# Performance work log

Measured on AMD Instinct MI355X. Metric: run time of the kernel, lower is better.

Reference implementation:

```python
import jax, jax.numpy as jnp
import numpy as np

H = 512          # hidden_dim
D = 128          # input_dim
L = 8            # output_dim == NUMLABELS
T = 64           # encoder time steps per frame-feature sequence
W = 240          # WINDOWWIDTH (encoder batch dim, one element per frame)
CTX = W // 4     # 60 attention positions
NSTEPS = W // 8


def _lstm(x, Wih, Whh, bih, bhh):
    """PyTorch-convention LSTM (gate order i,f,g,o). x: (T,B,Din) -> (outputs (T,B,H), final h (B,H))."""
    B = x.shape[1]
    Hh = Whh.shape[1]
    xp = jnp.einsum('tbd,gd->tbg', x, Wih) + bih + bhh  # fold both biases
    def step(carry, g):
        h, c = carry
        g = g + h @ Whh.T
        i, f, gg, o = jnp.split(g, 4, axis=-1)
        c = jax.nn.sigmoid(f) * c + jax.nn.sigmoid(i) * jnp.tanh(gg)
        h = jax.nn.sigmoid(o) * jnp.tanh(c)
        return (h, c), h
    z = jnp.zeros((B, Hh), x.dtype)
    (hT, _), hs = jax.lax.scan(step, (z, z), xp)
    return hs, hT


def _forward(data, enc_Wih, enc_Whh, enc_bih, enc_bhh,
             p1f_Wih, p1f_Whh, p1f_bih, p1f_bhh, p1b_Wih, p1b_Whh, p1b_bih, p1b_bhh,
             p2f_Wih, p2f_Whh, p2f_bih, p2f_bhh, p2b_Wih, p2b_Whh, p2b_bih, p2b_bhh,
             attn_W, attn_b, comb_W, comb_b,
             gru_Wih, gru_Whh, gru_bih, gru_bhh, out_W, out_b):
    # --- encoder: per-frame LSTM over T steps, keep final hidden per frame ---
    _, h_enc = _lstm(data, enc_Wih, enc_Whh, enc_bih, enc_bhh)          # (W, H)
    # --- pyramidal bi-LSTM 1: pairs of frames ---
    x1 = h_enc.reshape(W // 2, 1, 2 * H)
    f1, _ = _lstm(x1, p1f_Wih, p1f_Whh, p1f_bih, p1f_bhh)
    b1, _ = _lstm(x1[::-1], p1b_Wih, p1b_Whh, p1b_bih, p1b_bhh)
    # --- pyramidal bi-LSTM 2 ---
    x2 = jnp.concatenate([f1, b1[::-1]], axis=-1).reshape(W // 4, 1, 4 * H)
    f2, h2T = _lstm(x2, p2f_Wih, p2f_Whh, p2f_bih, p2f_bhh)
    b2, _ = _lstm(x2[::-1], p2b_Wih, p2b_Whh, p2b_bih, p2b_bhh)
    ctx = jnp.concatenate([f2, b2[::-1]], axis=-1).reshape(CTX, 2 * H)  # (60, 2H)
    h = h2T[0]                                   # forward-direction final hidden, (H,)
    inp0 = jnp.zeros((L,), data.dtype).at[L - 1].set(1.0)  # one_hot(NOLABEL)

    def dec_step(carry, _):
        inp, h = carry
        aw = jax.nn.softmax(attn_W @ jnp.concatenate([inp, h]) + attn_b)    # (60,)
        applied = aw @ ctx                                                   # (2H,)
        o = jax.nn.relu(comb_W @ jnp.concatenate([inp, applied]) + comb_b)  # (H,)
        # PyTorch GRU cell (gate order r,z,n)
        gi = gru_Wih @ o + gru_bih
        gh = gru_Whh @ h + gru_bhh
        ir, iz, inn = jnp.split(gi, 3)
        hr, hz, hn = jnp.split(gh, 3)
        r = jax.nn.sigmoid(ir + hr)
        z = jax.nn.sigmoid(iz + hz)
        n = jnp.tanh(inn + r * hn)
        h_new = (1.0 - z) * n + z * h
        logp = jax.nn.log_softmax(out_W @ h_new + out_b)                     # (L,)
        return (logp, h_new), logp  # prediction feeds back as next input (y=None path)

    _, outputs = jax.lax.scan(dec_step, (inp0, h), None, length=NSTEPS)
    return outputs  # (30, L)


def setup_inputs() -> dict:
    key = jax.random.key(0)
    ks = iter(jax.random.split(key, 64))
    def mk(*shape):
        return (jax.random.normal(next(ks), shape) * 0.05).astype(jnp.float32)
    d = {"data": jax.random.normal(next(ks), (T, W, D), dtype=jnp.float32)}
    d.update(enc_Wih=mk(4 * H, D), enc_Whh=mk(4 * H, H), enc_bih=mk(4 * H), enc_bhh=mk(4 * H))
    for p, din in (("p1f", 2 * H), ("p1b", 2 * H), ("p2f", 4 * H), ("p2b", 4 * H)):
        d[p + "_Wih"] = mk(4 * H, din)
        d[p + "_Whh"] = mk(4 * H, H)
        d[p + "_bih"] = mk(4 * H)
        d[p + "_bhh"] = mk(4 * H)
    d.update(attn_W=mk(CTX, H + L), attn_b=mk(CTX), comb_W=mk(H, 2 * H + L), comb_b=mk(H),
             gru_Wih=mk(3 * H, H), gru_Whh=mk(3 * H, H), gru_bih=mk(3 * H), gru_bhh=mk(3 * H),
             out_W=mk(L, H), out_b=mk(L))
    return d


def reference(data, enc_Wih, enc_Whh, enc_bih, enc_bhh,
              p1f_Wih, p1f_Whh, p1f_bih, p1f_bhh, p1b_Wih, p1b_Whh, p1b_bih, p1b_bhh,
              p2f_Wih, p2f_Whh, p2f_bih, p2f_bhh, p2b_Wih, p2b_Whh, p2b_bih, p2b_bhh,
              attn_W, attn_b, comb_W, comb_b,
              gru_Wih, gru_Whh, gru_bih, gru_bhh, out_W, out_b):
    return _forward(data, enc_Wih, enc_Whh, enc_bih, enc_bhh,
                    p1f_Wih, p1f_Whh, p1f_bih, p1f_bhh, p1b_Wih, p1b_Whh, p1b_bih, p1b_bhh,
                    p2f_Wih, p2f_Whh, p2f_bih, p2f_bhh, p2b_Wih, p2b_Whh, p2b_bih, p2b_bhh,
                    attn_W, attn_b, comb_W, comb_b,
                    gru_Wih, gru_Whh, gru_bih, gru_bhh, out_W, out_b)
```

## Files before the change

### kernel.cpp

```cpp
#include <hip/hip_runtime.h>
#include <math.h>


typedef __attribute__((ext_vector_type(8))) short short8;
typedef __attribute__((ext_vector_type(4))) float floatx4;
typedef unsigned long long ull;

__device__ __forceinline__ float sigf(float x) { return 1.f / (1.f + __expf(-x)); }
__device__ __forceinline__ float tanh_f(float x) {
    float e = __expf(2.f * x);
    return 1.f - 2.f / (e + 1.f);
}
__device__ __forceinline__ unsigned short f2b(float x) {
    unsigned u = __float_as_uint(x);
    unsigned r = (u + 0x7FFFu + ((u >> 16) & 1u)) >> 16;
    return (unsigned short)r;
}

__device__ __forceinline__ float gld(const float* p) {
    return __hip_atomic_load(p, __ATOMIC_RELAXED, __HIP_MEMORY_SCOPE_AGENT);
}
__device__ __forceinline__ void gst(float* p, float v) {
    __hip_atomic_store(p, v, __ATOMIC_RELAXED, __HIP_MEMORY_SCOPE_AGENT);
}
__device__ __forceinline__ ull gldll(const ull* p) {
    return __hip_atomic_load(p, __ATOMIC_RELAXED, __HIP_MEMORY_SCOPE_AGENT);
}
__device__ __forceinline__ void gstll(ull* p, ull v) {
    __hip_atomic_store(p, v, __ATOMIC_RELAXED, __HIP_MEMORY_SCOPE_AGENT);
}
__device__ __forceinline__ ull packfe(float d, int ep) {
    return ((ull)(unsigned)ep << 32) | (ull)__float_as_uint(d);
}
__device__ __forceinline__ float lowf(ull v) { return __uint_as_float((unsigned)v); }

__global__ void init_k(float* __restrict__ ws) {
    for (int i = blockIdx.x * blockDim.x + threadIdx.x; i < 256000; i += gridDim.x * blockDim.x)
        ws[i] = 0.f;
}

__global__ void __launch_bounds__(256, 1) enc_all(
    const float* __restrict__ data,
    const float* __restrict__ Wih, const float* __restrict__ Whh,
    const float* __restrict__ bih, const float* __restrict__ bhh,
    ull* __restrict__ hbufF,
    float* __restrict__ henc)
{
    __shared__ short act2[20 * 64 * 8];
    __shared__ float gw[4][640];
    __shared__ float cs[512];
    __shared__ short hw[4][16][8];
    __shared__ float biasL[4][4][8];

    const int tid = threadIdx.x;
    const int fg = blockIdx.x >> 4, ds = blockIdx.x & 15;
    const int w = tid >> 6, lane = tid & 63;
    const int n = lane & 15, q = lane >> 4;

    short8 bfrag[2][20];
#pragma unroll
    for (int nt = 0; nt < 2; ++nt) {
        int rr = nt * 16 + n;
        int g = rr >> 3, dp = rr & 7;
        int grow = g * 512 + ds * 32 + w * 8 + dp;
#pragma unroll
        for (int kt = 0; kt < 20; ++kt) {
            int k0 = kt * 32 + q * 8;
            const float* src = (k0 < 512) ? (Whh + (size_t)grow * 512 + k0)
                                          : (Wih + (size_t)grow * 128 + (k0 - 512));
            float4 lo = *(const float4*)src;
            float4 hi = *(const float4*)(src + 4);
            short8 bf;
            bf[0] = (short)f2b(lo.x); bf[1] = (short)f2b(lo.y);
            bf[2] = (short)f2b(lo.z); bf[3] = (short)f2b(lo.w);
            bf[4] = (short)f2b(hi.x); bf[5] = (short)f2b(hi.y);
            bf[6] = (short)f2b(hi.z); bf[7] = (short)f2b(hi.w);
            bfrag[nt][kt] = bf;
        }
    }
    if (tid < 128) {
        int w2 = tid >> 5, rr = tid & 31;
        int g = rr >> 3, dp = rr & 7;
        int grow = g * 512 + ds * 32 + w2 * 8 + dp;
        biasL[w2][g][dp] = bih[grow] + bhh[grow];
    }
    for (int i = tid; i < 512; i += 256) cs[i] = 0.f;
    __syncthreads();

    unsigned* a2u = (unsigned*)act2;

    for (int t = 0; t < 64; ++t) {
        const int kt2 = tid >> 6, l2 = tid & 63, f2v = l2 & 15, q2 = l2 >> 4;
        const float* xs = data + ((size_t)t * 240 + fg * 16 + f2v) * 128 + kt2 * 32 + q2 * 8;
        float4 lo = *(const float4*)xs;
        float4 hi = *(const float4*)(xs + 4);

        {
            const ull* hsrc = hbufF + (size_t)((t & 1) * 15 + fg) * 4096;
            ull v[16];
            for (;;) {
                bool ok = true;
#pragma unroll
                for (int k2 = 0; k2 < 16; ++k2) {
                    v[k2] = gldll(hsrc + tid + 256 * k2);
                    ok &= ((int)(v[k2] >> 32) == t);
                }
                if (ok) break;
                __builtin_amdgcn_s_sleep(1);
            }
#pragma unroll
            for (int k2 = 0; k2 < 16; ++k2)
                a2u[tid + 256 * k2] = (unsigned)v[k2];
        }
        {
            short8 xp;
            xp[0] = (short)f2b(lo.x); xp[1] = (short)f2b(lo.y);
            xp[2] = (short)f2b(lo.z); xp[3] = (short)f2b(lo.w);
            xp[4] = (short)f2b(hi.x); xp[5] = (short)f2b(hi.y);
            xp[6] = (short)f2b(hi.z); xp[7] = (short)f2b(hi.w);
            *(short8*)&act2[((16 + kt2) * 64 + l2) * 8] = xp;
        }
        __syncthreads();

        floatx4 acc0 = {0.f, 0.f, 0.f, 0.f};
        floatx4 acc1 = {0.f, 0.f, 0.f, 0.f};
#pragma unroll
        for (int kt = 0; kt < 20; ++kt) {
            short8 a = *(short8*)&act2[(kt * 64 + lane) * 8];
            acc0 = __builtin_amdgcn_mfma_f32_16x16x32_bf16(a, bfrag[0][kt], acc0, 0, 0, 0);
            acc1 = __builtin_amdgcn_mfma_f32_16x16x32_bf16(a, bfrag[1][kt], acc1, 0, 0, 0);
        }
        *(floatx4*)&gw[w][(0 * 16 + n) * 20 + 4 * q] = acc0;
        *(floatx4*)&gw[w][(1 * 16 + n) * 20 + 4 * q] = acc1;

        int nb = (t + 1) & 1;
#pragma unroll
        for (int it = 0; it < 2; ++it) {
            int f = lane & 15, dp = q + 4 * it;
            float gi = gw[w][(0 * 8 + dp) * 20 + f] + biasL[w][0][dp];
            float gf = gw[w][(1 * 8 + dp) * 20 + f] + biasL[w][1][dp];
            float gg = gw[w][(2 * 8 + dp) * 20 + f] + biasL[w][2][dp];
            float go = gw[w][(3 * 8 + dp) * 20 + f] + biasL[w][3][dp];
            int ci = f * 32 + w * 8 + dp;
            float cc = cs[ci];
            float cn = sigf(gf) * cc + sigf(gi) * tanh_f(gg);
            float hn = sigf(go) * tanh_f(cn);
            cs[ci] = cn;
            hw[w][f][dp] = (short)f2b(hn);
            if (t == 63)
                gst(&henc[(size_t)(fg * 16 + f) * 512 + ds * 32 + w * 8 + dp], hn);
        }
        if (lane < 16) {
            const unsigned* hwu = (const unsigned*)&hw[w][lane][0];
            ull* dst = hbufF + (size_t)(nb * 15 + fg) * 4096 + (ds * 64 + w * 16 + lane) * 4;
            const ull ep = ((ull)(unsigned)(t + 1)) << 32;
#pragma unroll
            for (int r = 0; r < 4; ++r)
                gstll(dst + r, ep | (ull)hwu[r]);
        }
        __syncthreads();
    }
}

__global__ void __launch_bounds__(256) gemm_xp2(
    const float* __restrict__ A, int M, int K, int halfgrid,
    const float* __restrict__ WvF, const float* __restrict__ baF,
    const float* __restrict__ bbF, float* __restrict__ CF,
    const float* __restrict__ WvB, const float* __restrict__ baB,
    const float* __restrict__ bbB, float* __restrict__ CB)
{
    __shared__ float At[16][66];
    __shared__ float Wt[128][66];
    const int tid = threadIdx.x;
    int bgl = blockIdx.x;
    const int rev = (bgl >= halfgrid) ? 1 : 0;
    if (rev) bgl -= halfgrid;
    const float* Wv = rev ? WvB : WvF;
    const float* ba = rev ? baB : baF;
    const float* bb = rev ? bbB : bbF;
    float* C        = rev ? CB : CF;

    const int nt = bgl & 15, mt = bgl >> 4;
    const int rp = tid >> 2, fq = tid & 3;
    const int lr0 = 2 * rp, lr1 = lr0 + 1;
    const int n0 = nt * 128 + lr0, n1 = n0 + 1;

    float acc0[4], acc1[4];
    {
        float b0 = ba[n0] + bb[n0], b1 = ba[n1] + bb[n1];
#pragma unroll
        for (int j = 0; j < 4; ++j) { acc0[j] = b0; acc1[j] = b1; }
    }

    for (int kt = 0; kt < K; kt += 64) {
        {
            int f = tid >> 4, c4 = tid & 15;
            int m = mt * 16 + f;
            float4 v = make_float4(0.f, 0.f, 0.f, 0.f);
            if (m < M) {
                int ar = rev ? (M - 1 - m) : m;
                v = ((const float4*)(A + (size_t)ar * K + kt))[c4];
            }
            At[f][c4 * 4 + 0] = v.x; At[f][c4 * 4 + 1] = v.y;
            At[f][c4 * 4 + 2] = v.z; At[f][c4 * 4 + 3] = v.w;
        }
        for (int i = tid; i < 2048; i += 256) {
            int lr = i >> 4, c4 = i & 15;
            float4 v = ((const float4*)(Wv + (size_t)(nt * 128 + lr) * K + kt))[c4];
            Wt[lr][c4 * 4 + 0] = v.x; Wt[lr][c4 * 4 + 1] = v.y;
            Wt[lr][c4 * 4 + 2] = v.z; Wt[lr][c4 * 4 + 3] = v.w;
        }
        __syncthreads();
        const float2* w0p = (const float2*)(&Wt[lr0][0]);
        const float2* w1p = (const float2*)(&Wt[lr1][0]);
#pragma unroll 8
        for (int kh = 0; kh < 32; ++kh) {
            float2 w0 = w0p[kh], w1 = w1p[kh];
#pragma unroll
            for (int j = 0; j < 4; ++j) {
                float2 av = ((const float2*)(&At[4 * fq + j][0]))[kh];
                acc0[j] += w0.x * av.x + w0.y * av.y;
                acc1[j] += w1.x * av.x + w1.y * av.y;
            }
        }
        __syncthreads();
    }
#pragma unroll
    for (int j = 0; j < 4; ++j) {
        int m = mt * 16 + 4 * fq + j;
        if (m < M) {
            C[(size_t)m * 2048 + n0] = acc0[j];
            C[(size_t)m * 2048 + n1] = acc1[j];
        }
    }
}

__global__ void __launch_bounds__(256, 1) pyr_rec(
    const float* __restrict__ xpF, const float* __restrict__ xpB,
    const float* __restrict__ WhhF, const float* __restrict__ WhhB,
    ull* __restrict__ hp,
    float* __restrict__ outF, float* __restrict__ outB,
    int steps)
{
    const int tid = threadIdx.x;
    const int dir = blockIdx.x >> 6, blk = blockIdx.x & 63;
    const float* xp  = dir ? xpB : xpF;
    const float* Whh = dir ? WhhB : WhhF;
    float* outp = dir ? outB : outF;
    ull* hpd = hp + (size_t)dir * 1024;

    __shared__ __align__(16) float hcur[512];
    __shared__ float red[32][9];
    __shared__ float gv[32];

    const int lr = tid & 31, seg = tid >> 5;
    const int grow = (lr >> 3) * 512 + blk * 8 + (lr & 7);
    float4 wl4[16];
#pragma unroll
    for (int j = 0; j < 16; ++j)
        wl4[j] = *(const float4*)&Whh[(size_t)grow * 512 + 4 * seg + 32 * j];

    const int growx = (tid >> 3) * 512 + blk * 8 + (tid & 7);
    float creg = 0.f;
    __syncthreads();

    for (int t = 0; t < steps; ++t) {
        float xg = 0.f;
        if (tid < 32) xg = xp[(size_t)t * 2048 + growx];
        {
            const ull* base = hpd + (size_t)(t & 1) * 512;
            ull v0 = gldll(base + tid), v1 = gldll(base + tid + 256);
            while (((int)(v0 >> 32) != t) | ((int)(v1 >> 32) != t)) {
                __builtin_amdgcn_s_sleep(1);
                v0 = gldll(base + tid);
                v1 = gldll(base + tid + 256);
            }
            hcur[tid]       = lowf(v0);
            hcur[tid + 256] = lowf(v1);
        }
        __syncthreads();

        float a = 0.f;
#pragma unroll
        for (int j = 0; j < 16; ++j) {
            float4 w = wl4[j];
            float4 h4 = *(const float4*)&hcur[4 * seg + 32 * j];
            a += w.x*h4.x + w.y*h4.y + w.z*h4.z + w.w*h4.w;
        }
        red[lr][seg] = a;
        __syncthreads();

        if (tid < 32) {
            float g = xg;
#pragma unroll
            for (int s2 = 0; s2 < 8; ++s2) g += red[tid][s2];
            gv[tid] = g;
        }
        __syncthreads();
        if (tid < 8) {
            float i_ = sigf(gv[tid]), f_ = sigf(gv[8 + tid]);
            float g_ = tanh_f(gv[16 + tid]), o_ = sigf(gv[24 + tid]);
            creg = f_ * creg + i_ * g_;
            float hn = o_ * tanh_f(creg);
            int d = blk * 8 + tid;
            gstll(&hpd[((t + 1) & 1) * 512 + d], packfe(hn, t + 1));
            int row = dir ? (steps - 1 - t) : t;
            outp[(size_t)row * 512 + d] = hn;
        }
        __syncthreads();
    }
}

__global__ void x2_assemble(const float* __restrict__ f1, const float* __restrict__ b1o,
                            float* __restrict__ x2)
{
    int j = blockIdx.x;
    for (int k = threadIdx.x; k < 2048; k += 256) {
        int q = k >> 9, r = k & 511;
        const float* src = (q & 1) ? b1o : f1;
        int row = 2 * j + (q >> 1);
        x2[(size_t)j * 2048 + k] = src[(size_t)row * 512 + r];
    }
}

__global__ void ctx_k(const float* __restrict__ f2, const float* __restrict__ b2o,
                      float* __restrict__ ctx, ull* __restrict__ hdec_p)
{
    int j = blockIdx.x;
    for (int k = threadIdx.x; k < 1024; k += 256)
        ctx[(size_t)j * 1024 + k] = (k < 512) ? f2[(size_t)j * 512 + k]
                                              : b2o[(size_t)j * 512 + k - 512];
    if (j == 0) {
        for (int i = threadIdx.x; i < 512; i += 256)
            hdec_p[i] = packfe(f2[59 * 512 + i], 0);
    }
}

__global__ void __launch_bounds__(256) precomp_M(
    const float* __restrict__ comb_W,
    const float* __restrict__ ctx,
    float* __restrict__ MgT)
{
    __shared__ float cw[8 * 1024];
    const int tid = threadIdx.x, d0 = blockIdx.x * 8;
    for (int i = tid; i < 2048; i += 256) {
        int r = i >> 8, c4 = i & 255;
        float4 v = *(const float4*)&comb_W[(size_t)(d0 + r) * 1032 + 8 + 4 * c4];
        *(float4*)&cw[r * 1024 + 4 * c4] = v;
    }
    __syncthreads();
    for (int o = tid; o < 480; o += 256) {
        int dl = o / 60, j = o % 60;
        const float4* cp = (const float4*)&cw[dl * 1024];
        const float4* xp = (const float4*)(ctx + (size_t)j * 1024);
        float a = 0.f;
#pragma unroll 4
        for (int k = 0; k < 256; ++k) {
            float4 w = cp[k], x = xp[k];
            a += w.x * x.x + w.y * x.y + w.z * x.z + w.w * x.w;
        }
        MgT[(size_t)j * 512 + (d0 + dl)] = a;
    }
}

__global__ void __launch_bounds__(512, 1) dec_k(
    const float* __restrict__ attn_W, const float* __restrict__ attn_b,
    const float* __restrict__ comb_W, const float* __restrict__ comb_b,
    const float* __restrict__ gWih, const float* __restrict__ gWhh,
    const float* __restrict__ gbih, const float* __restrict__ gbhh,
    const float* __restrict__ outW, const float* __restrict__ outb,
    const float* __restrict__ MgT,
    ull* __restrict__ hdec_p,
    float* __restrict__ dout)
{
    const int tid = threadIdx.x, bid = blockIdx.x;
    const int lane = tid & 63, wv = tid >> 6;
    const int dbase = bid * 8;

    __shared__ float M2T[68][512];
    __shared__ __align__(16) float hL[520];
    __shared__ __align__(16) float xl[512];
    __shared__ __align__(16) float awx[68];
    __shared__ float zd[8], zh[64];
    __shared__ float ghl[24], gil[24];
    __shared__ float biasg[24], biasi[24];
    __shared__ float cbL[512];
    __shared__ float attnbL[64], outbL[8];

    const int rg = tid >> 4, sg = tid & 15;
    const int rz = tid >> 3, szz = tid & 7;

    float4 wo2[2];
    float4 wg8[8], wi8[8];
    float4 wzh[16];
    float4 wip[2];
    {
        const float* wp = outW + (size_t)wv * 512 + 4 * lane;
        wo2[0] = *(const float4*)wp;
        wo2[1] = *(const float4*)(wp + 256);
    }
    {
        int rr = (rg < 24) ? rg : 23;
        size_t grow = (size_t)((rr >> 3) * 512 + dbase + (rr & 7)) * 512 + 4 * sg;
#pragma unroll
        for (int i = 0; i < 8; ++i) {
            wg8[i] = *(const float4*)&gWhh[grow + 64 * i];
            wi8[i] = *(const float4*)&gWih[grow + 64 * i];
        }
    }
    {
        int rr = (rz < 60) ? rz : 59;
        size_t base = (size_t)rr * 520 + 8 + 4 * szz;
#pragma unroll
        for (int i = 0; i < 16; ++i)
            wzh[i] = *(const float4*)&attn_W[base + 32 * i];
    }
    {
        int rr = (tid < 60) ? tid : 59;
        wip[0] = *(const float4*)&attn_W[(size_t)rr * 520 + 0];
        wip[1] = *(const float4*)&attn_W[(size_t)rr * 520 + 4];
    }
    if (tid < 24) {
        int g2 = (tid >> 3) * 512 + dbase + (tid & 7);
        biasg[tid] = gbhh[g2];
        biasi[tid] = gbih[g2];
    }
    cbL[tid] = comb_b[tid];
    if (tid < 64) attnbL[tid] = (tid < 60) ? attn_b[tid] : 0.f;
    if (tid < 8) outbL[tid] = outb[tid];
    for (int i = tid; i < 7680; i += 512) {
        int j = i >> 7, c4 = i & 127;
        *(float4*)&M2T[j][4 * c4] = *(const float4*)&MgT[(size_t)j * 512 + 4 * c4];
    }
    for (int i = tid; i < 4096; i += 512) {
        int r = i >> 3, c = i & 7;
        M2T[60 + c][r] = comb_W[(size_t)r * 1032 + c];
    }
    __syncthreads();

    for (int s = 0; s < 30; ++s) {
        {
            const ull* hs = hdec_p + (size_t)(s & 1) * 512;
            ull v0 = gldll(hs + tid);
            while ((int)(v0 >> 32) != s) {
                __builtin_amdgcn_s_sleep(1);
                v0 = gldll(hs + tid);
            }
            hL[tid] = lowf(v0);
        }
        __syncthreads();

        {
            float a = 0.f;
            float4 h0 = *(const float4*)&hL[4 * lane];
            float4 h1 = *(const float4*)&hL[4 * lane + 256];
            a += wo2[0].x*h0.x + wo2[0].y*h0.y + wo2[0].z*h0.z + wo2[0].w*h0.w;
            a += wo2[1].x*h1.x + wo2[1].y*h1.y + wo2[1].z*h1.z + wo2[1].w*h1.w;
#pragma unroll
            for (int off = 32; off; off >>= 1) a += __shfl_xor(a, off);
            if (lane == 0) zd[wv] = a;
        }
        {
            float a = 0.f;
#pragma unroll
            for (int i = 0; i < 8; ++i) {
                float4 w = wg8[i];
                float4 h4 = *(const float4*)&hL[4 * sg + 64 * i];
                a += w.x*h4.x + w.y*h4.y + w.z*h4.z + w.w*h4.w;
            }
            a += __shfl_xor(a, 1); a += __shfl_xor(a, 2);
            a += __shfl_xor(a, 4); a += __shfl_xor(a, 8);
            if (sg == 0 && rg < 24) ghl[rg] = a;
        }
        {
            float a = 0.f;
#pragma unroll
            for (int i = 0; i < 16; ++i) {
                float4 w = wzh[i];
                float4 h4 = *(const float4*)&hL[4 * szz + 32 * i];
                a += w.x*h4.x + w.y*h4.y + w.z*h4.z + w.w*h4.w;
            }
            a += __shfl_xor(a, 1); a += __shfl_xor(a, 2); a += __shfl_xor(a, 4);
            if (szz == 0 && rz < 60) zh[rz] = a;
        }
        __syncthreads();

        if (wv == 0) {
            if (lane < 8) {
                float v;
                if (s > 0) {
                    float a = zd[lane] + outbL[lane];
                    float m = a;
                    m = fmaxf(m, __shfl_xor(m, 1));
                    m = fmaxf(m, __shfl_xor(m, 2));
                    m = fmaxf(m, __shfl_xor(m, 4));
                    float e = __expf(a - m);
                    float ss2 = e;
                    ss2 += __shfl_xor(ss2, 1);
                    ss2 += __shfl_xor(ss2, 2);
                    ss2 += __shfl_xor(ss2, 4);
                    v = a - m - __logf(ss2);
                    if (bid == 0) dout[(s - 1) * 8 + lane] = v;
                } else {
                    v = (lane == 7) ? 1.f : 0.f;
                }
                awx[60 + lane] = v;
            }
            float z = -1e30f;
            if (lane < 60) {
                z = zh[lane] + attnbL[lane]
                  + wip[0].x * awx[60] + wip[0].y * awx[61]
                  + wip[0].z * awx[62] + wip[0].w * awx[63]
                  + wip[1].x * awx[64] + wip[1].y * awx[65]
                  + wip[1].z * awx[66] + wip[1].w * awx[67];
            }
            float m = z;
#pragma unroll
            for (int off = 32; off; off >>= 1) m = fmaxf(m, __shfl_xor(m, off));
            float e = (lane < 60) ? __expf(z - m) : 0.f;
            float ss2 = e;
#pragma unroll
            for (int off = 32; off; off >>= 1) ss2 += __shfl_xor(ss2, off);
            if (lane < 60) awx[lane] = e / ss2;
        }
        __syncthreads();

        {
            float a = cbL[tid];
#pragma unroll 4
            for (int k = 0; k < 68; ++k)
                a += M2T[k][tid] * awx[k];
            xl[tid] = fmaxf(a, 0.f);
        }
        __syncthreads();

        {
            float a = 0.f;
#pragma unroll
            for (int i = 0; i < 8; ++i) {
                float4 w = wi8[i];
                float4 o4 = *(const float4*)&xl[4 * sg + 64 * i];
                a += w.x*o4.x + w.y*o4.y + w.z*o4.z + w.w*o4.w;
            }
            a += __shfl_xor(a, 1); a += __shfl_xor(a, 2);
            a += __shfl_xor(a, 4); a += __shfl_xor(a, 8);
            if (sg == 0 && rg < 24) gil[rg] = a;
        }
        __syncthreads();

        if (tid < 8) {
            float gh0 = biasg[tid] + ghl[tid];
            float gh1 = biasg[8 + tid] + ghl[8 + tid];
            float gh2 = biasg[16 + tid] + ghl[16 + tid];
            float gi0 = biasi[tid] + gil[tid];
            float gi1 = biasi[8 + tid] + gil[8 + tid];
            float gi2 = biasi[16 + tid] + gil[16 + tid];
            float r_ = sigf(gi0 + gh0);
            float z_ = sigf(gi1 + gh1);
            float n_ = tanh_f(gi2 + r_ * gh2);
            float hnew = (1.f - z_) * n_ + z_ * hL[dbase + tid];
            gstll(&hdec_p[(size_t)((s + 1) & 1) * 512 + dbase + tid], packfe(hnew, s + 1));
        }
        __syncthreads();
    }

    if (bid == 0) {
        {
            const ull* hs = hdec_p + (size_t)(30 & 1) * 512;
            ull v0 = gldll(hs + tid);
            while ((int)(v0 >> 32) != 30) {
                __builtin_amdgcn_s_sleep(1);
                v0 = gldll(hs + tid);
            }
            hL[tid] = lowf(v0);
        }
        __syncthreads();
        {
            float a = 0.f;
            float4 h0 = *(const float4*)&hL[4 * lane];
            float4 h1 = *(const float4*)&hL[4 * lane + 256];
            a += wo2[0].x*h0.x + wo2[0].y*h0.y + wo2[0].z*h0.z + wo2[0].w*h0.w;
            a += wo2[1].x*h1.x + wo2[1].y*h1.y + wo2[1].z*h1.z + wo2[1].w*h1.w;
#pragma unroll
            for (int off = 32; off; off >>= 1) a += __shfl_xor(a, off);
            if (lane == 0) zd[wv] = a;
        }
        __syncthreads();
        if (tid < 8) {
            float a = zd[tid] + outbL[tid];
            float m = a;
            m = fmaxf(m, __shfl_xor(m, 1));
            m = fmaxf(m, __shfl_xor(m, 2));
            m = fmaxf(m, __shfl_xor(m, 4));
            float e = __expf(a - m);
            float ss2 = e;
            ss2 += __shfl_xor(ss2, 1);
            ss2 += __shfl_xor(ss2, 2);
            ss2 += __shfl_xor(ss2, 4);
            dout[29 * 8 + tid] = a - m - __logf(ss2);
        }
    }
}

extern "C" void kernel_launch(void* const* d_in, const int* in_sizes, int n_in,
                              void* d_out, int out_size, void* d_ws, size_t ws_size,
                              hipStream_t stream) {
    (void)in_sizes; (void)n_in; (void)out_size; (void)ws_size;
    const float* data    = (const float*)d_in[0];
    const float* enc_Wih = (const float*)d_in[1];
    const float* enc_Whh = (const float*)d_in[2];
    const float* enc_bih = (const float*)d_in[3];
    const float* enc_bhh = (const float*)d_in[4];
    const float* p1f_Wih = (const float*)d_in[5];
    const float* p1f_Whh = (const float*)d_in[6];
    const float* p1f_bih = (const float*)d_in[7];
    const float* p1f_bhh = (const float*)d_in[8];
    const float* p1b_Wih = (const float*)d_in[9];
    const float* p1b_Whh = (const float*)d_in[10];
    const float* p1b_bih = (const float*)d_in[11];
    const float* p1b_bhh = (const float*)d_in[12];
    const float* p2f_Wih = (const float*)d_in[13];
    const float* p2f_Whh = (const float*)d_in[14];
    const float* p2f_bih = (const float*)d_in[15];
    const float* p2f_bhh = (const float*)d_in[16];
    const float* p2b_Wih = (const float*)d_in[17];
    const float* p2b_Whh = (const float*)d_in[18];
    const float* p2b_bih = (const float*)d_in[19];
    const float* p2b_bhh = (const float*)d_in[20];
    const float* attn_W  = (const float*)d_in[21];
    const float* attn_b  = (const float*)d_in[22];
    const float* comb_W  = (const float*)d_in[23];
    const float* comb_b  = (const float*)d_in[24];
    const float* gru_Wih = (const float*)d_in[25];
    const float* gru_Whh = (const float*)d_in[26];
    const float* gru_bih = (const float*)d_in[27];
    const float* gru_bhh = (const float*)d_in[28];
    const float* out_W   = (const float*)d_in[29];
    const float* out_b   = (const float*)d_in[30];

    float* ws = (float*)d_ws;
    ull* hbufF   = (ull*)ws;
    ull* hp1     = (ull*)(ws + 245760);
    ull* hp2     = (ull*)(ws + 249856);
    ull* hdec_p  = (ull*)(ws + 253952);
    float* henc  = ws + 256000;
    float* xp1f  = ws + 378880;
    float* xp1b  = ws + 624640;
    float* f1    = ws + 870400;
    float* b1o   = ws + 931840;
    float* x2    = ws + 993280;
    float* xp2f  = ws + 1116160;
    float* xp2b  = ws + 1239040;
    float* f2    = ws + 1361920;
    float* b2o   = ws + 1392640;
    float* ctxb  = ws + 1423360;
    float* MgT   = ws + 1484800;

    init_k<<<256, 256, 0, stream>>>(ws);

    enc_all<<<240, 256, 0, stream>>>(data, enc_Wih, enc_Whh, enc_bih, enc_bhh,
                                     hbufF, henc);
    gemm_xp2<<<256, 256, 0, stream>>>(henc, 120, 1024, 128,
                                      p1f_Wih, p1f_bih, p1f_bhh, xp1f,
                                      p1b_Wih, p1b_bih, p1b_bhh, xp1b);
    pyr_rec<<<128, 256, 0, stream>>>(xp1f, xp1b, p1f_Whh, p1b_Whh, hp1, f1, b1o, 120);
    x2_assemble<<<60, 256, 0, stream>>>(f1, b1o, x2);
    gemm_xp2<<<128, 256, 0, stream>>>(x2, 60, 2048, 64,
                                      p2f_Wih, p2f_bih, p2f_bhh, xp2f,
                                      p2b_Wih, p2b_bih, p2b_bhh, xp2b);
    pyr_rec<<<128, 256, 0, stream>>>(xp2f, xp2b, p2f_Whh, p2b_Whh, hp2, f2, b2o, 60);
    ctx_k<<<60, 256, 0, stream>>>(f2, b2o, ctxb, hdec_p);
    precomp_M<<<64, 256, 0, stream>>>(comb_W, ctxb, MgT);
    dec_k<<<64, 512, 0, stream>>>(attn_W, attn_b, comb_W, comb_b,
                                  gru_Wih, gru_Whh, gru_bih, gru_bhh,
                                  out_W, out_b, MgT, hdec_p,
                                  (float*)d_out);
}
```

Baseline: 1.192 ms.

## Remap encoder blocks by XCD and add a fast L2-local hidden-state exchange path

```diff
diff --git a/kernel.cpp b/kernel.cpp
--- a/kernel.cpp
+++ b/kernel.cpp
@@ -35,7 +35,7 @@
 __device__ __forceinline__ float lowf(ull v) { return __uint_as_float((unsigned)v); }
 
 __global__ void init_k(float* __restrict__ ws) {
-    for (int i = blockIdx.x * blockDim.x + threadIdx.x; i < 256000; i += gridDim.x * blockDim.x)
+    for (int i = blockIdx.x * blockDim.x + threadIdx.x; i < 501760; i += gridDim.x * blockDim.x)
         ws[i] = 0.f;
 }
 
@@ -43,6 +43,7 @@
     const float* __restrict__ data,
     const float* __restrict__ Wih, const float* __restrict__ Whh,
     const float* __restrict__ bih, const float* __restrict__ bhh,
+    ull* __restrict__ fastF,
     ull* __restrict__ hbufF,
     float* __restrict__ henc)
 {
@@ -53,7 +54,10 @@
     __shared__ float biasL[4][4][8];
 
     const int tid = threadIdx.x;
-    const int fg = blockIdx.x >> 4, ds = blockIdx.x & 15;
+    const int xcd = blockIdx.x & 7, kk = blockIdx.x >> 3;
+    const int fg = xcd * 2 + (kk >> 4), ds = kk & 15;
+    if (fg >= 15) return;
+
     const int w = tid >> 6, lane = tid & 63;
     const int n = lane & 15, q = lane >> 4;
 
@@ -96,13 +100,22 @@
         float4 hi = *(const float4*)(xs + 4);
 
         {
-            const ull* hsrc = hbufF + (size_t)((t & 1) * 15 + fg) * 4096;
+            const size_t goff = (size_t)((t & 1) * 15 + fg) * 4096;
+            const ull* fsrc = fastF + goff;
+            const ull* ssrc = hbufF + goff;
             ull v[16];
             for (;;) {
                 bool ok = true;
 #pragma unroll
                 for (int k2 = 0; k2 < 16; ++k2) {
-                    v[k2] = gldll(hsrc + tid + 256 * k2);
+                    v[k2] = *(volatile const ull*)(fsrc + tid + 256 * k2);
+                    ok &= ((int)(v[k2] >> 32) == t);
+                }
+                if (ok) break;
+                ok = true;
+#pragma unroll
+                for (int k2 = 0; k2 < 16; ++k2) {
+                    v[k2] = gldll(ssrc + tid + 256 * k2);
                     ok &= ((int)(v[k2] >> 32) == t);
                 }
                 if (ok) break;
@@ -152,11 +165,16 @@
         }
         if (lane < 16) {
             const unsigned* hwu = (const unsigned*)&hw[w][lane][0];
-            ull* dst = hbufF + (size_t)(nb * 15 + fg) * 4096 + (ds * 64 + w * 16 + lane) * 4;
+            size_t off = (size_t)(nb * 15 + fg) * 4096 + (ds * 64 + w * 16 + lane) * 4;
+            ull* fdst = fastF + off;
+            ull* sdst = hbufF + off;
             const ull ep = ((ull)(unsigned)(t + 1)) << 32;
 #pragma unroll
-            for (int r = 0; r < 4; ++r)
-                gstll(dst + r, ep | (ull)hwu[r]);
+            for (int r = 0; r < 4; ++r) {
+                ull wv = ep | (ull)hwu[r];
+                *(volatile ull*)(fdst + r) = wv;
+                gstll(sdst + r, wv);
+            }
         }
         __syncthreads();
     }
@@ -639,27 +657,28 @@
     const float* out_b   = (const float*)d_in[30];
 
     float* ws = (float*)d_ws;
-    ull* hbufF   = (ull*)ws;
-    ull* hp1     = (ull*)(ws + 245760);
-    ull* hp2     = (ull*)(ws + 249856);
-    ull* hdec_p  = (ull*)(ws + 253952);
-    float* henc  = ws + 256000;
-    float* xp1f  = ws + 378880;
-    float* xp1b  = ws + 624640;
-    float* f1    = ws + 870400;
-    float* b1o   = ws + 931840;
-    float* x2    = ws + 993280;
-    float* xp2f  = ws + 1116160;
-    float* xp2b  = ws + 1239040;
-    float* f2    = ws + 1361920;
-    float* b2o   = ws + 1392640;
-    float* ctxb  = ws + 1423360;
-    float* MgT   = ws + 1484800;
+    ull* fastF   = (ull*)ws;
+    ull* hbufF   = (ull*)(ws + 245760);
+    ull* hp1     = (ull*)(ws + 491520);
+    ull* hp2     = (ull*)(ws + 495616);
+    ull* hdec_p  = (ull*)(ws + 499712);
+    float* henc  = ws + 501760;
+    float* xp1f  = ws + 624640;
+    float* xp1b  = ws + 870400;
+    float* f1    = ws + 1116160;
+    float* b1o   = ws + 1177600;
+    float* x2    = ws + 1239040;
+    float* xp2f  = ws + 1361920;
+    float* xp2b  = ws + 1484800;
+    float* f2    = ws + 1607680;
+    float* b2o   = ws + 1638400;
+    float* ctxb  = ws + 1669120;
+    float* MgT   = ws + 1730560;
 
     init_k<<<256, 256, 0, stream>>>(ws);
 
-    enc_all<<<240, 256, 0, stream>>>(data, enc_Wih, enc_Whh, enc_bih, enc_bhh,
-                                     hbufF, henc);
+    enc_all<<<256, 256, 0, stream>>>(data, enc_Wih, enc_Whh, enc_bih, enc_bhh,
+                                     fastF, hbufF, henc);
     gemm_xp2<<<256, 256, 0, stream>>>(henc, 120, 1024, 128,
                                       p1f_Wih, p1f_bih, p1f_bhh, xp1f,
                                       p1b_Wih, p1b_bih, p1b_bhh, xp1b);
```

Result: slower. 1.442 ms (+21.0%).

## Fuse x2/ctx assembly into consumers and use shuffle reduction in pyr_rec

Applied to the files above, without the earlier changes.

```diff
diff --git a/kernel.cpp b/kernel.cpp
--- a/kernel.cpp
+++ b/kernel.cpp
@@ -235,6 +235,84 @@
     }
 }
 
+__global__ void __launch_bounds__(256) gemm_x2(
+    const float* __restrict__ f1, const float* __restrict__ b1o,
+    int M, int K, int halfgrid,
+    const float* __restrict__ WvF, const float* __restrict__ baF,
+    const float* __restrict__ bbF, float* __restrict__ CF,
+    const float* __restrict__ WvB, const float* __restrict__ baB,
+    const float* __restrict__ bbB, float* __restrict__ CB)
+{
+    __shared__ float At[16][66];
+    __shared__ float Wt[128][66];
+    const int tid = threadIdx.x;
+    int bgl = blockIdx.x;
+    const int rev = (bgl >= halfgrid) ? 1 : 0;
+    if (rev) bgl -= halfgrid;
+    const float* Wv = rev ? WvB : WvF;
+    const float* ba = rev ? baB : baF;
+    const float* bb = rev ? bbB : bbF;
+    float* C        = rev ? CB : CF;
+
+    const int nt = bgl & 15, mt = bgl >> 4;
+    const int rp = tid >> 2, fq = tid & 3;
+    const int lr0 = 2 * rp, lr1 = lr0 + 1;
+    const int n0 = nt * 128 + lr0, n1 = n0 + 1;
+
+    float acc0[4], acc1[4];
+    {
+        float b0 = ba[n0] + bb[n0], b1 = ba[n1] + bb[n1];
+#pragma unroll
+        for (int j = 0; j < 4; ++j) { acc0[j] = b0; acc1[j] = b1; }
+    }
+
+    for (int kt = 0; kt < K; kt += 64) {
+        {
+            int f = tid >> 4, c4 = tid & 15;
+            int m = mt * 16 + f;
+            float4 v = make_float4(0.f, 0.f, 0.f, 0.f);
+            if (m < M) {
+                int ar = rev ? (M - 1 - m) : m;
+                int seg = kt >> 9;
+                int r = (kt & 511) + 4 * c4;
+                const float* src = (seg & 1) ? b1o : f1;
+                int srow = 2 * ar + (seg >> 1);
+                v = *(const float4*)&src[(size_t)srow * 512 + r];
+            }
+            At[f][c4 * 4 + 0] = v.x; At[f][c4 * 4 + 1] = v.y;
+            At[f][c4 * 4 + 2] = v.z; At[f][c4 * 4 + 3] = v.w;
+        }
+        for (int i = tid; i < 2048; i += 256) {
+            int lr = i >> 4, c4 = i & 15;
+            float4 v = ((const float4*)(Wv + (size_t)(nt * 128 + lr) * K + kt))[c4];
+            Wt[lr][c4 * 4 + 0] = v.x; Wt[lr][c4 * 4 + 1] = v.y;
+            Wt[lr][c4 * 4 + 2] = v.z; Wt[lr][c4 * 4 + 3] = v.w;
+        }
+        __syncthreads();
+        const float2* w0p = (const float2*)(&Wt[lr0][0]);
+        const float2* w1p = (const float2*)(&Wt[lr1][0]);
+#pragma unroll 8
+        for (int kh = 0; kh < 32; ++kh) {
+            float2 w0 = w0p[kh], w1 = w1p[kh];
+#pragma unroll
+            for (int j = 0; j < 4; ++j) {
+                float2 av = ((const float2*)(&At[4 * fq + j][0]))[kh];
+                acc0[j] += w0.x * av.x + w0.y * av.y;
+                acc1[j] += w1.x * av.x + w1.y * av.y;
+            }
+        }
+        __syncthreads();
+    }
+#pragma unroll
+    for (int j = 0; j < 4; ++j) {
+        int m = mt * 16 + 4 * fq + j;
+        if (m < M) {
+            C[(size_t)m * 2048 + n0] = acc0[j];
+            C[(size_t)m * 2048 + n1] = acc1[j];
+        }
+    }
+}
+
 __global__ void __launch_bounds__(256, 1) pyr_rec(
     const float* __restrict__ xpF, const float* __restrict__ xpB,
     const float* __restrict__ WhhF, const float* __restrict__ WhhB,
@@ -250,23 +328,21 @@
     ull* hpd = hp + (size_t)dir * 1024;
 
     __shared__ __align__(16) float hcur[512];
-    __shared__ float red[32][9];
     __shared__ float gv[32];
 
-    const int lr = tid & 31, seg = tid >> 5;
-    const int grow = (lr >> 3) * 512 + blk * 8 + (lr & 7);
+    const int row = tid >> 3, seg = tid & 7;
+    const int grow = (row >> 3) * 512 + blk * 8 + (row & 7);
     float4 wl4[16];
 #pragma unroll
     for (int j = 0; j < 16; ++j)
         wl4[j] = *(const float4*)&Whh[(size_t)grow * 512 + 4 * seg + 32 * j];
 
-    const int growx = (tid >> 3) * 512 + blk * 8 + (tid & 7);
     float creg = 0.f;
     __syncthreads();
 
     for (int t = 0; t < steps; ++t) {
         float xg = 0.f;
-        if (tid < 32) xg = xp[(size_t)t * 2048 + growx];
+        if (seg == 0) xg = xp[(size_t)t * 2048 + grow];
         {
             const ull* base = hpd + (size_t)(t & 1) * 512;
             ull v0 = gldll(base + tid), v1 = gldll(base + tid + 256);
@@ -287,16 +363,12 @@
             float4 h4 = *(const float4*)&hcur[4 * seg + 32 * j];
             a += w.x*h4.x + w.y*h4.y + w.z*h4.z + w.w*h4.w;
         }
-        red[lr][seg] = a;
-        __syncthreads();
-
-        if (tid < 32) {
-            float g = xg;
-#pragma unroll
-            for (int s2 = 0; s2 < 8; ++s2) g += red[tid][s2];
-            gv[tid] = g;
-        }
-        __syncthreads();
+        a += __shfl_xor(a, 1);
+        a += __shfl_xor(a, 2);
+        a += __shfl_xor(a, 4);
+        if (seg == 0) gv[row] = a + xg;
+        __syncthreads();
+
         if (tid < 8) {
             float i_ = sigf(gv[tid]), f_ = sigf(gv[8 + tid]);
             float g_ = tanh_f(gv[16 + tid]), o_ = sigf(gv[24 + tid]);
@@ -304,42 +376,19 @@
             float hn = o_ * tanh_f(creg);
             int d = blk * 8 + tid;
             gstll(&hpd[((t + 1) & 1) * 512 + d], packfe(hn, t + 1));
-            int row = dir ? (steps - 1 - t) : t;
-            outp[(size_t)row * 512 + d] = hn;
-        }
-        __syncthreads();
-    }
-}
-
-__global__ void x2_assemble(const float* __restrict__ f1, const float* __restrict__ b1o,
-                            float* __restrict__ x2)
-{
-    int j = blockIdx.x;
-    for (int k = threadIdx.x; k < 2048; k += 256) {
-        int q = k >> 9, r = k & 511;
-        const float* src = (q & 1) ? b1o : f1;
-        int row = 2 * j + (q >> 1);
-        x2[(size_t)j * 2048 + k] = src[(size_t)row * 512 + r];
-    }
-}
-
-__global__ void ctx_k(const float* __restrict__ f2, const float* __restrict__ b2o,
-                      float* __restrict__ ctx, ull* __restrict__ hdec_p)
-{
-    int j = blockIdx.x;
-    for (int k = threadIdx.x; k < 1024; k += 256)
-        ctx[(size_t)j * 1024 + k] = (k < 512) ? f2[(size_t)j * 512 + k]
-                                              : b2o[(size_t)j * 512 + k - 512];
-    if (j == 0) {
-        for (int i = threadIdx.x; i < 512; i += 256)
-            hdec_p[i] = packfe(f2[59 * 512 + i], 0);
+            int row2 = dir ? (steps - 1 - t) : t;
+            outp[(size_t)row2 * 512 + d] = hn;
+        }
+        __syncthreads();
     }
 }
 
 __global__ void __launch_bounds__(256) precomp_M(
     const float* __restrict__ comb_W,
-    const float* __restrict__ ctx,
-    float* __restrict__ MgT)
+    const float* __restrict__ f2,
+    const float* __restrict__ b2o,
+    float* __restrict__ MgT,
+    ull* __restrict__ hdec_p)
 {
     __shared__ float cw[8 * 1024];
     const int tid = threadIdx.x, d0 = blockIdx.x * 8;
@@ -348,15 +397,26 @@
         float4 v = *(const float4*)&comb_W[(size_t)(d0 + r) * 1032 + 8 + 4 * c4];
         *(float4*)&cw[r * 1024 + 4 * c4] = v;
     }
+    if (blockIdx.x == 0) {
+        for (int i = tid; i < 512; i += 256)
+            hdec_p[i] = packfe(f2[59 * 512 + i], 0);
+    }
     __syncthreads();
     for (int o = tid; o < 480; o += 256) {
         int dl = o / 60, j = o % 60;
-        const float4* cp = (const float4*)&cw[dl * 1024];
-        const float4* xp = (const float4*)(ctx + (size_t)j * 1024);
+        const float4* cp0 = (const float4*)&cw[dl * 1024];
+        const float4* cp1 = (const float4*)&cw[dl * 1024 + 512];
+        const float4* xf = (const float4*)(f2 + (size_t)j * 512);
+        const float4* xb = (const float4*)(b2o + (size_t)j * 512);
         float a = 0.f;
 #pragma unroll 4
-        for (int k = 0; k < 256; ++k) {
-            float4 w = cp[k], x = xp[k];
+        for (int k = 0; k < 128; ++k) {
+            float4 w = cp0[k], x = xf[k];
+            a += w.x * x.x + w.y * x.y + w.z * x.z + w.w * x.w;
+        }
+#pragma unroll 4
+        for (int k = 0; k < 128; ++k) {
+            float4 w = cp1[k], x = xb[k];
             a += w.x * x.x + w.y * x.y + w.z * x.z + w.w * x.w;
         }
         MgT[(size_t)j * 512 + (d0 + dl)] = a;
@@ -648,13 +708,11 @@
     float* xp1b  = ws + 624640;
     float* f1    = ws + 870400;
     float* b1o   = ws + 931840;
-    float* x2    = ws + 993280;
-    float* xp2f  = ws + 1116160;
-    float* xp2b  = ws + 1239040;
-    float* f2    = ws + 1361920;
-    float* b2o   = ws + 1392640;
-    float* ctxb  = ws + 1423360;
-    float* MgT   = ws + 1484800;
+    float* xp2f  = ws + 993280;
+    float* xp2b  = ws + 1116160;
+    float* f2    = ws + 1239040;
+    float* b2o   = ws + 1269760;
+    float* MgT   = ws + 1300480;
 
     init_k<<<256, 256, 0, stream>>>(ws);
 
@@ -664,13 +722,11 @@
                                       p1f_Wih, p1f_bih, p1f_bhh, xp1f,
                                       p1b_Wih, p1b_bih, p1b_bhh, xp1b);
     pyr_rec<<<128, 256, 0, stream>>>(xp1f, xp1b, p1f_Whh, p1b_Whh, hp1, f1, b1o, 120);
-    x2_assemble<<<60, 256, 0, stream>>>(f1, b1o, x2);
-    gemm_xp2<<<128, 256, 0, stream>>>(x2, 60, 2048, 64,
-                                      p2f_Wih, p2f_bih, p2f_bhh, xp2f,
-                                      p2b_Wih, p2b_bih, p2b_bhh, xp2b);
+    gemm_x2<<<128, 256, 0, stream>>>(f1, b1o, 60, 2048, 64,
+                                     p2f_Wih, p2f_bih, p2f_bhh, xp2f,
+                                     p2b_Wih, p2b_bih, p2b_bhh, xp2b);
     pyr_rec<<<128, 256, 0, stream>>>(xp2f, xp2b, p2f_Whh, p2b_Whh, hp2, f2, b2o, 60);
-    ctx_k<<<60, 256, 0, stream>>>(f2, b2o, ctxb, hdec_p);
-    precomp_M<<<64, 256, 0, stream>>>(comb_W, ctxb, MgT);
+    precomp_M<<<64, 256, 0, stream>>>(comb_W, f2, b2o, MgT, hdec_p);
     dec_k<<<64, 512, 0, stream>>>(attn_W, attn_b, comb_W, comb_b,
                                   gru_Wih, gru_Whh, gru_bih, gru_bhh,
                                   out_W, out_b, MgT, hdec_p,
```

After: 1.198 ms. About the same (+0.5%).
